# Kernel tuning notes

Measured on AMD Instinct MI355X. Metric: run time of the kernel, lower is better.

The kernel has to match this reference:

```python
import jax, jax.numpy as jnp
import numpy as np

FACTOR = 3   # ProbAttention factor hardcoded in Informer.__init__
N_HEADS = 8


def _ln(x, g, b, eps=1e-5):
    m = x.mean(-1, keepdims=True)
    v = ((x - m) ** 2).mean(-1, keepdims=True)
    return (x - m) / jnp.sqrt(v + eps) * g + b


def _pos_emb(L, d_model):
    # standard fixed sinusoidal positional embedding (Informer PositionalEmbedding)
    pos = np.arange(L, dtype=np.float32)[:, None]
    div = np.exp(np.arange(0, d_model, 2, dtype=np.float32) * (-np.log(10000.0) / d_model))
    pe = np.zeros((L, d_model), np.float32)
    pe[:, 0::2] = np.sin(pos * div)
    pe[:, 1::2] = np.cos(pos * div)
    return jnp.asarray(pe)


def _prob_attention(q, k, v, rng_key):
    # q,k,v: [B, L, H, D]; mask_flag=False, scale=None -> 1/sqrt(D)
    B, L, H, D = q.shape
    Q = q.transpose(0, 2, 1, 3)
    K = k.transpose(0, 2, 1, 3)
    V = v.transpose(0, 2, 1, 3)
    L_Q = L_K = L
    U_part = min(FACTOR * int(np.ceil(np.log(L_K))), L_K)   # sampled keys per query
    u = min(FACTOR * int(np.ceil(np.log(L_Q))), L_Q)        # top queries kept
    # sample keys (shared across batch/heads, as in torch.randint(L_K,(L_Q,sample_k)))
    idx_sample = jax.random.randint(rng_key, (L_Q, U_part), 0, L_K)
    K_sample = K[:, :, idx_sample, :]                        # [B,H,L_Q,U_part,D]
    QK_sample = jnp.einsum('bhld,bhlsd->bhls', Q, K_sample)  # [B,H,L_Q,U_part]
    M = QK_sample.max(-1) - QK_sample.sum(-1) / L_K          # sparsity measure [B,H,L_Q]
    _, idx_top = jax.lax.top_k(M, u)                         # [B,H,u]
    Q_reduce = jnp.take_along_axis(Q, idx_top[..., None], axis=2)          # [B,H,u,D]
    scores = jnp.einsum('bhud,bhkd->bhuk', Q_reduce, K) / jnp.sqrt(jnp.float32(D))
    attn = jax.nn.softmax(scores, axis=-1)
    upd = jnp.einsum('bhuk,bhkd->bhud', attn, V)             # [B,H,u,D]
    # initial context = mean over values (mask_flag=False), overwrite at top queries
    ctx = jnp.broadcast_to(V.mean(axis=2, keepdims=True), (B, H, L_Q, D))
    bI = jnp.arange(B)[:, None, None]
    hI = jnp.arange(H)[None, :, None]
    ctx = ctx.at[bI, hI, idx_top].set(upd)
    return ctx.transpose(0, 2, 1, 3).reshape(B, L, H * D)


def _forward(x, time_features, g_in, b_in, W_tok, W_time, b_time,
             Wq, bq, Wk, bk, Wv, bv, Wo, bo, W1, b1, W2, b2,
             g1, be1, g2, be2, g_enc, b_enc, W_pre, b_pre, W_fc, b_fc):
    B, L, _ = x.shape
    d_model = W_tok.shape[-1]
    H = N_HEADS
    D = d_model // H
    x = _ln(x, g_in, b_in)                                   # input_norm over enc_in
    # DataEmbedding: circular Conv1d(k=3) token emb + positional + timeF linear
    xp = jnp.pad(x, ((0, 0), (1, 1), (0, 0)), mode='wrap')
    tok = jax.lax.conv_general_dilated(xp, W_tok, (1,), 'VALID',
                                       dimension_numbers=('NWC', 'WIO', 'NWC'))
    h = tok + _pos_emb(L, d_model)[None] + time_features @ W_time.T + b_time
    key = jax.random.key(42)
    for i in range(Wq.shape[0]):                              # e_layers (small, fixed)
        q = (h @ Wq[i].T + bq[i]).reshape(B, L, H, D)
        k = (h @ Wk[i].T + bk[i]).reshape(B, L, H, D)
        v = (h @ Wv[i].T + bv[i]).reshape(B, L, H, D)
        attn_out = _prob_attention(q, k, v, jax.random.fold_in(key, i))
        h = h + attn_out @ Wo[i].T + bo[i]
        h = _ln(h, g1[i], be1[i])
        y = jax.nn.relu(h @ W1[i].T + b1[i]) @ W2[i].T + b2[i]  # 1x1 convs == linears
        h = _ln(h + y, g2[i], be2[i])
    h = _ln(h, g_enc, b_enc)
    last = h[:, -1, :]
    return jax.nn.relu(last @ W_pre.T + b_pre) @ W_fc.T + b_fc


def setup_inputs() -> dict:
    key = jax.random.key(0)
    B, L, C_IN, DM, DFF, E = 8, 2048, 32, 512, 2048, 2
    ks = iter(jax.random.split(key, 48))

    def p(shape, s=0.02):
        return jax.random.normal(next(ks), shape, jnp.float32) * s

    return {
        'x': jax.random.normal(next(ks), (B, L, C_IN), jnp.float32),
        'time_features': jax.random.uniform(next(ks), (B, L, 4), jnp.float32),
        'g_in': jnp.ones((C_IN,), jnp.float32), 'b_in': jnp.zeros((C_IN,), jnp.float32),
        'W_tok': p((3, C_IN, DM)),
        'W_time': p((DM, 4)), 'b_time': jnp.zeros((DM,), jnp.float32),
        'Wq': p((E, DM, DM)), 'bq': jnp.zeros((E, DM), jnp.float32),
        'Wk': p((E, DM, DM)), 'bk': jnp.zeros((E, DM), jnp.float32),
        'Wv': p((E, DM, DM)), 'bv': jnp.zeros((E, DM), jnp.float32),
        'Wo': p((E, DM, DM)), 'bo': jnp.zeros((E, DM), jnp.float32),
        'W1': p((E, DFF, DM)), 'b1': jnp.zeros((E, DFF), jnp.float32),
        'W2': p((E, DM, DFF)), 'b2': jnp.zeros((E, DM), jnp.float32),
        'g1': jnp.ones((E, DM), jnp.float32), 'be1': jnp.zeros((E, DM), jnp.float32),
        'g2': jnp.ones((E, DM), jnp.float32), 'be2': jnp.zeros((E, DM), jnp.float32),
        'g_enc': jnp.ones((DM,), jnp.float32), 'b_enc': jnp.zeros((DM,), jnp.float32),
        'W_pre': p((DM // 2, DM)), 'b_pre': jnp.zeros((DM // 2,), jnp.float32),
        'W_fc': p((1, DM // 2)), 'b_fc': jnp.zeros((1,), jnp.float32),
    }


def reference(x, time_features, g_in, b_in, W_tok, W_time, b_time,
              Wq, bq, Wk, bk, Wv, bv, Wo, bo, W1, b1, W2, b2,
              g1, be1, g2, be2, g_enc, b_enc, W_pre, b_pre, W_fc, b_fc):
    return _forward(x, time_features, g_in, b_in, W_tok, W_time, b_time,
                    Wq, bq, Wk, bk, Wv, bv, Wo, bo, W1, b1, W2, b2,
                    g1, be1, g2, be2, g_enc, b_enc, W_pre, b_pre, W_fc, b_fc)
```

## Files before the change

kernel.cpp:

```cpp
#include <hip/hip_runtime.h>
#include <math.h>

#define BATCH 8
#define SEQ   2048
#define TOK   (BATCH*SEQ)
#define CIN   32
#define DM    512
#define DFF   2048
#define NH    8
#define HD    64
#define NSAMP 24
#define NTOP  24
#define EPS   1e-5f
#define QKVLD 1536

typedef unsigned int u32;
typedef unsigned short u16;
typedef unsigned long long u64;
typedef __attribute__((ext_vector_type(8))) short short8;
typedef __attribute__((ext_vector_type(4))) short short4v;
typedef __attribute__((ext_vector_type(4))) float floatx4;

__device__ __forceinline__ void async16(const void* g, void* l) {
    __builtin_amdgcn_global_load_lds((const __attribute__((address_space(1))) u32*)g,
                                     (__attribute__((address_space(3))) u32*)l, 16, 0, 0);
}
__device__ __forceinline__ u16 bf16rn(float f) {
    u32 u = __float_as_uint(f);
    return (u16)((u + 0x7fffu + ((u >> 16) & 1u)) >> 16);
}
__device__ __forceinline__ void sep_store(u16* base, size_t row, int ld2, int j, float v) {
    u16 hb = bf16rn(v);
    float r = v - __uint_as_float((u32)hb << 16);
    size_t o = row * (size_t)ld2 + (size_t)((j >> 3) << 4) + (j & 7);
    base[o] = hb;
    base[o + 8] = bf16rn(r);
}
__device__ __forceinline__ float sep_load(const u16* base, size_t row, int ld2, int j) {
    size_t o = row * (size_t)ld2 + (size_t)((j >> 3) << 4) + (j & 7);
    return __uint_as_float((u32)base[o] << 16) + __uint_as_float((u32)base[o + 8] << 16);
}
__device__ __forceinline__ float hl2f(u16 h, u16 l) {
    return __uint_as_float((u32)h << 16) + __uint_as_float((u32)l << 16);
}

__device__ __forceinline__ void tf_round(unsigned &x0, unsigned &x1, int r) {
    x0 += x1;
    x1 = (x1 << r) | (x1 >> (32 - r));
    x1 ^= x0;
}
__device__ __forceinline__ void threefry(unsigned k0, unsigned k1,
                                         unsigned c0, unsigned c1,
                                         unsigned &o0, unsigned &o1) {
    unsigned ks0 = k0, ks1 = k1, ks2 = k0 ^ k1 ^ 0x1BD11BDAu;
    unsigned x0 = c0 + ks0, x1 = c1 + ks1;
    tf_round(x0,x1,13); tf_round(x0,x1,15); tf_round(x0,x1,26); tf_round(x0,x1,6);
    x0 += ks1; x1 += ks2 + 1u;
    tf_round(x0,x1,17); tf_round(x0,x1,29); tf_round(x0,x1,16); tf_round(x0,x1,24);
    x0 += ks2; x1 += ks0 + 2u;
    tf_round(x0,x1,13); tf_round(x0,x1,15); tf_round(x0,x1,26); tf_round(x0,x1,6);
    x0 += ks0; x1 += ks1 + 3u;
    tf_round(x0,x1,17); tf_round(x0,x1,29); tf_round(x0,x1,16); tf_round(x0,x1,24);
    x0 += ks1; x1 += ks2 + 4u;
    tf_round(x0,x1,13); tf_round(x0,x1,15); tf_round(x0,x1,26); tf_round(x0,x1,6);
    x0 += ks2; x1 += ks0 + 5u;
    o0 = x0; o1 = x1;
}

__global__ void sample_kernel(int* __restrict__ idx_sample) {
    const int HALF = (SEQ * NSAMP) / 2;
    int p = blockIdx.x * blockDim.x + threadIdx.x;
    int li = blockIdx.y;
    if (p >= HALF) return;
    unsigned f0, f1;
    threefry(0u, 42u, 0u, (unsigned)li, f0, f1);
    unsigned a0, a1, b0, b1;
    threefry(f0, f1, 0u, 2u, a0, a1);
    threefry(f0, f1, 1u, 3u, b0, b1);
    unsigned o0, o1;
    threefry(a1, b1, (unsigned)p, (unsigned)(p + HALF), o0, o1);
    idx_sample[li * SEQ * NSAMP + p]        = (int)(o0 & (SEQ - 1));
    idx_sample[li * SEQ * NSAMP + p + HALF] = (int)(o1 & (SEQ - 1));
}

__global__ __launch_bounds__(256) void ln_in_kernel(const float* __restrict__ x,
        const float* __restrict__ g, const float* __restrict__ b,
        float* __restrict__ out) {
    int t = blockIdx.x * blockDim.x + threadIdx.x;
    if (t >= TOK) return;
    const float* xr = x + (size_t)t * CIN;
    float vals[CIN];
    float s = 0.f;
#pragma unroll
    for (int c = 0; c < CIN; c++) { vals[c] = xr[c]; s += vals[c]; }
    float m = s * (1.f / CIN);
    float v = 0.f;
#pragma unroll
    for (int c = 0; c < CIN; c++) { float d = vals[c] - m; v += d * d; }
    v *= (1.f / CIN);
    float inv = rsqrtf(v + EPS);
    float* orow = out + (size_t)t * CIN;
#pragma unroll
    for (int c = 0; c < CIN; c++) orow[c] = (vals[c] - m) * inv * g[c] + b[c];
}

__global__ __launch_bounds__(128) void im2col_kernel(const float* __restrict__ xln,
        u16* __restrict__ a) {
    int t = blockIdx.x;
    int j = threadIdx.x;
    if (j >= 96) return;
    int b = t >> 11, l = t & 2047;
    int w = j >> 5, c = j & 31;
    int lw = (l - 1 + w + SEQ) & 2047;
    sep_store(a, (size_t)t, 192, j, xln[(((size_t)b << 11) | lw) * CIN + c]);
}

__global__ __launch_bounds__(256) void wtok_split(const float* __restrict__ Wtok,
        u16* __restrict__ wt) {
    int e = blockIdx.x * 256 + threadIdx.x;
    int o = e / 96, j = e % 96;
    sep_store(wt, (size_t)o, 192, j, Wtok[(size_t)j * DM + o]);
}

__global__ __launch_bounds__(256) void pe_kernel(float* __restrict__ pe) {
    int e = blockIdx.x * 256 + threadIdx.x;
    int l = e >> 9, o = e & 511;
    const float c1 = -0.017988946039016f;
    int i2 = o & ~1;
    float div = expf((float)i2 * c1);
    float arg = (float)l * div;
    pe[e] = (o & 1) ? cosf(arg) : sinf(arg);
}

__global__ __launch_bounds__(256) void rsd_kernel(const float* __restrict__ pe,
        const float* __restrict__ tfeat, const float* __restrict__ Wtime,
        u16* __restrict__ rsd) {
    int t = blockIdx.x, tid = threadIdx.x;
    int l = t & 2047;
    float t0 = tfeat[(size_t)t * 4], t1 = tfeat[(size_t)t * 4 + 1];
    float t2 = tfeat[(size_t)t * 4 + 2], t3 = tfeat[(size_t)t * 4 + 3];
    for (int o = tid; o < DM; o += 256) {
        float v = pe[l * DM + o]
            + t0 * Wtime[o * 4] + t1 * Wtime[o * 4 + 1]
            + t2 * Wtime[o * 4 + 2] + t3 * Wtime[o * 4 + 3];
        sep_store(rsd, (size_t)t, 1024, o, v);
    }
}

__global__ __launch_bounds__(256) void split_weights(const float* __restrict__ Wq,
        const float* __restrict__ Wk, const float* __restrict__ Wv,
        const float* __restrict__ Wo, const float* __restrict__ W1,
        const float* __restrict__ W2, u16* __restrict__ out,
        const float* __restrict__ bq, const float* __restrict__ bk,
        const float* __restrict__ bv, float* __restrict__ bqkv) {
    int i = blockIdx.x * 256 + threadIdx.x;
    if (i < 1536)
        bqkv[i] = (i < 512) ? bq[i] : (i < 1024) ? bk[i - 512] : bv[i - 1024];
    if (i < 1048576) {
        const float* src = (i < 262144) ? Wq : (i < 524288) ? Wk : (i < 786432) ? Wv : Wo;
        int off = i & 262143;
        size_t base = (size_t)(i >> 18) * 524288;
        sep_store(out + base, (size_t)(off >> 9), 1024, off & 511, src[off]);
    } else if (i < 2097152) {
        int off = i - 1048576;
        sep_store(out + 2097152, (size_t)(off >> 9), 1024, off & 511, W1[off]);
    } else {
        int off = i - 2097152;
        sep_store(out + 4194304, (size_t)(off >> 11), 4096, off & 2047, W2[off]);
    }
}

template<bool RELU, bool RESP, bool OUTP, bool OUTB>
__global__ __launch_bounds__(256, 2) void gemm_pp(const u16* __restrict__ Ap,
        const u16* __restrict__ Wp, const float* __restrict__ bias,
        const u16* __restrict__ RsdS, float* __restrict__ Cf, u16* __restrict__ Cp,
        int ldc, int K, int lda) {
    __shared__ alignas(16) u16 At[2][8192];
    __shared__ alignas(16) u16 Wt[2][8192];
    const int tid = threadIdx.x;
    int linear = blockIdx.y * gridDim.x + blockIdx.x;
    int xcd = linear & 7, sseq = linear >> 3;
    int mper = gridDim.y >> 3;
    int mt = xcd * mper + (sseq % mper);
    int nt = sseq / mper;
    const int m0 = mt * 128, n0 = nt * 128;
    const int lane = tid & 63, wv = tid >> 6;
    const int wm = wv >> 1, wn = wv & 1;
    const int fr = lane & 15, q = lane >> 4;

    floatx4 acc[4][4] = {};

    const int r0 = tid >> 3;
    const int gc = (tid & 7) ^ (r0 & 7);
    const u16* abase = Ap + (size_t)(m0 + r0) * (2 * lda) + gc * 8;
    const u16* wbase = Wp + (size_t)(n0 + r0) * (2 * K) + gc * 8;
    const size_t astep = (size_t)32 * 2 * lda;
    const size_t wstep = (size_t)32 * 2 * K;
    const int doff = tid * 16;
    const int nk = K >> 5;

    const int cph = ((q << 1) ^ (fr & 7)) << 3;
    const int cpl = ((q << 1) ^ (fr & 7) ^ 1) << 3;

#pragma unroll
    for (int i = 0; i < 4; i++) {
        async16(abase + i * astep, (char*)At[0] + doff + i * 4096);
        async16(wbase + i * wstep, (char*)Wt[0] + doff + i * 4096);
    }

    for (int k = 0; k < nk; k++) {
        const int b = k & 1;
        __syncthreads();
        if (k + 1 < nk) {
            int k2 = (k + 1) << 6;
#pragma unroll
            for (int i = 0; i < 4; i++) {
                async16(abase + k2 + i * astep, (char*)At[b ^ 1] + doff + i * 4096);
                async16(wbase + k2 + i * wstep, (char*)Wt[b ^ 1] + doff + i * 4096);
            }
        }
        short8 ah[4], al[4];
#pragma unroll
        for (int mi = 0; mi < 4; mi++) {
            int r = wm * 64 + mi * 16 + fr;
            ah[mi] = *(const short8*)&At[b][r * 64 + cph];
            al[mi] = *(const short8*)&At[b][r * 64 + cpl];
        }
#pragma unroll
        for (int ni = 0; ni < 4; ni++) {
            int r = wn * 64 + ni * 16 + fr;
            short8 wh8 = *(const short8*)&Wt[b][r * 64 + cph];
            short8 wl8 = *(const short8*)&Wt[b][r * 64 + cpl];
#pragma unroll
            for (int mi = 0; mi < 4; mi++) {
                acc[mi][ni] = __builtin_amdgcn_mfma_f32_16x16x32_bf16(ah[mi], wh8, acc[mi][ni], 0, 0, 0);
                acc[mi][ni] = __builtin_amdgcn_mfma_f32_16x16x32_bf16(ah[mi], wl8, acc[mi][ni], 0, 0, 0);
                acc[mi][ni] = __builtin_amdgcn_mfma_f32_16x16x32_bf16(al[mi], wh8, acc[mi][ni], 0, 0, 0);
            }
        }
    }
#pragma unroll
    for (int ni = 0; ni < 4; ni++) {
        int col = n0 + wn * 64 + ni * 16 + fr;
        float bv = bias[col];
#pragma unroll
        for (int mi = 0; mi < 4; mi++) {
            int row = m0 + wm * 64 + mi * 16 + q * 4;
#pragma unroll
            for (int r = 0; r < 4; r++) {
                float v = acc[mi][ni][r] + bv;
                if (RESP) v += sep_load(RsdS, (size_t)(row + r), 2 * ldc, col);
                if (RELU) v = fmaxf(v, 0.f);
                if (OUTP)      sep_store(Cp, (size_t)(row + r), 2 * ldc, col, v);
                else if (OUTB) Cp[(size_t)(row + r) * ldc + col] = bf16rn(v);
                else           Cf[(size_t)(row + r) * ldc + col] = v;
            }
        }
    }
}

template<bool RELU, bool RESP>
__global__ __launch_bounds__(256, 2) void gemm_sb(const u16* __restrict__ Ab,
        const u16* __restrict__ Wp, const float* __restrict__ bias,
        const u16* __restrict__ RsdS, float* __restrict__ Cf,
        int ldc, int K, int lda) {
    __shared__ alignas(16) u16 At[2][4096];
    __shared__ alignas(16) u16 Wt[2][8192];
    const int tid = threadIdx.x;
    int linear = blockIdx.y * gridDim.x + blockIdx.x;
    int xcd = linear & 7, sseq = linear >> 3;
    int mper = gridDim.y >> 3;
    int mt = xcd * mper + (sseq % mper);
    int nt = sseq / mper;
    const int m0 = mt * 128, n0 = nt * 128;
    const int lane = tid & 63, wv = tid >> 6;
    const int wm = wv >> 1, wn = wv & 1;
    const int fr = lane & 15, q = lane >> 4;

    floatx4 acc[4][4] = {};

    const int ar = tid & 127;
    const u16* abase = Ab + (size_t)(m0 + ar) * lda + (tid >> 7) * 8;
    const int adoff = tid * 16;
    const int r0 = tid >> 3;
    const int gc = (tid & 7) ^ (r0 & 7);
    const u16* wbase = Wp + (size_t)(n0 + r0) * (2 * K) + gc * 8;
    const size_t wstep = (size_t)32 * 2 * K;
    const int wdoff = tid * 16;
    const int nk = K >> 5;

    const int cph = ((q << 1) ^ (fr & 7)) << 3;
    const int cpl = ((q << 1) ^ (fr & 7) ^ 1) << 3;

#pragma unroll
    for (int i = 0; i < 2; i++)
        async16(abase + i * 16, (char*)At[0] + adoff + i * 4096);
#pragma unroll
    for (int i = 0; i < 4; i++)
        async16(wbase + i * wstep, (char*)Wt[0] + wdoff + i * 4096);

    for (int k = 0; k < nk; k++) {
        const int b = k & 1;
        __syncthreads();
        if (k + 1 < nk) {
            int ka = (k + 1) << 5;
            int kw = (k + 1) << 6;
#pragma unroll
            for (int i = 0; i < 2; i++)
                async16(abase + ka + i * 16, (char*)At[b ^ 1] + adoff + i * 4096);
#pragma unroll
            for (int i = 0; i < 4; i++)
                async16(wbase + kw + i * wstep, (char*)Wt[b ^ 1] + wdoff + i * 4096);
        }
        short8 af[4];
#pragma unroll
        for (int mi = 0; mi < 4; mi++) {
            int r = wm * 64 + mi * 16 + fr;
            af[mi] = *(const short8*)&At[b][q * 1024 + r * 8];
        }
#pragma unroll
        for (int ni = 0; ni < 4; ni++) {
            int r = wn * 64 + ni * 16 + fr;
            short8 wh8 = *(const short8*)&Wt[b][r * 64 + cph];
            short8 wl8 = *(const short8*)&Wt[b][r * 64 + cpl];
#pragma unroll
            for (int mi = 0; mi < 4; mi++) {
                acc[mi][ni] = __builtin_amdgcn_mfma_f32_16x16x32_bf16(af[mi], wh8, acc[mi][ni], 0, 0, 0);
                acc[mi][ni] = __builtin_amdgcn_mfma_f32_16x16x32_bf16(af[mi], wl8, acc[mi][ni], 0, 0, 0);
            }
        }
    }
#pragma unroll
    for (int ni = 0; ni < 4; ni++) {
        int col = n0 + wn * 64 + ni * 16 + fr;
        float bv = bias[col];
#pragma unroll
        for (int mi = 0; mi < 4; mi++) {
            int row = m0 + wm * 64 + mi * 16 + q * 4;
#pragma unroll
            for (int r = 0; r < 4; r++) {
                float v = acc[mi][ni][r] + bv;
                if (RESP) v += sep_load(RsdS, (size_t)(row + r), 2 * ldc, col);
                if (RELU) v = fmaxf(v, 0.f);
                Cf[(size_t)(row + r) * ldc + col] = v;
            }
        }
    }
}

__global__ __launch_bounds__(256) void qk_sample_kernel(const float* __restrict__ qkv,
        const int* __restrict__ idx_sample, float* __restrict__ Mout) {
    int r = (blockIdx.x * 256 + threadIdx.x) >> 6;
    int lane = threadIdx.x & 63;
    if (r >= BATCH * NH * SEQ) return;
    int b = r / (NH * SEQ);
    int head = (r / SEQ) % NH;
    int l = r % SEQ;
    int sidx = lane >> 4, dc = lane & 15;
    const float* qrow = qkv + ((size_t)(b * SEQ + l)) * QKVLD + head * HD + dc * 4;
    float4 qf = *(const float4*)qrow;
    int myidx = (lane < NSAMP) ? idx_sample[l * NSAMP + lane] : 0;
    const float* kbase = qkv + (size_t)b * SEQ * QKVLD + 512 + head * HD + dc * 4;
    int kidx[6];
#pragma unroll
    for (int p = 0; p < 6; p++) kidx[p] = __shfl(myidx, p * 4 + sidx);
    float4 kf[6];
#pragma unroll
    for (int p = 0; p < 6; p++) kf[p] = *(const float4*)(kbase + (size_t)kidx[p] * QKVLD);
    float mx = -INFINITY, sm = 0.f;
#pragma unroll
    for (int p = 0; p < 6; p++) {
        float part = qf.x * kf[p].x + qf.y * kf[p].y + qf.z * kf[p].z + qf.w * kf[p].w;
        part += __shfl_xor(part, 1);
        part += __shfl_xor(part, 2);
        part += __shfl_xor(part, 4);
        part += __shfl_xor(part, 8);
        mx = fmaxf(mx, part);
        sm += part;
    }
    mx = fmaxf(mx, __shfl_xor(mx, 16));
    mx = fmaxf(mx, __shfl_xor(mx, 32));
    sm += __shfl_xor(sm, 16);
    sm += __shfl_xor(sm, 32);
    if (lane == 0) Mout[r] = mx - sm * (1.f / SEQ);
}

__device__ __forceinline__ u64 pack_key(float v, int idx) {
    u32 u = __float_as_uint(v);
    u32 m = (u & 0x80000000u) ? ~u : (u | 0x80000000u);
    return ((u64)m << 32) | (u32)(~(u32)idx);
}

__global__ __launch_bounds__(256) void topk_part(const float* __restrict__ Mbuf,
        u64* __restrict__ cand) {
    __shared__ u64 wred[4];
    int bh = blockIdx.x, chunk = blockIdx.y;
    int tid = threadIdx.x, wv = tid >> 6, lane = tid & 63;
    int l = chunk * 256 + tid;
    u64 val = pack_key(Mbuf[(size_t)bh * SEQ + l], l);
    for (int it = 0; it < NTOP; it++) {
        u64 w = val;
#pragma unroll
        for (int off = 32; off > 0; off >>= 1) {
            u64 o = __shfl_xor(w, off);
            if (o > w) w = o;
        }
        if (lane == 0) wred[wv] = w;
        __syncthreads();
        u64 win = wred[0];
        if (wred[1] > win) win = wred[1];
        if (wred[2] > win) win = wred[2];
        if (wred[3] > win) win = wred[3];
        if (val == win) val = 0;
        if (tid == 0) cand[((size_t)bh * 8 + chunk) * NTOP + it] = win;
        __syncthreads();
    }
}

__global__ __launch_bounds__(256) void topk_merge(const u64* __restrict__ cand,
        int* __restrict__ idx_top) {
    __shared__ u64 wred[4];
    int bh = blockIdx.x;
    int tid = threadIdx.x, wv = tid >> 6, lane = tid & 63;
    u64 val = (tid < 8 * NTOP) ? cand[(size_t)bh * 8 * NTOP + tid] : 0;
    for (int it = 0; it < NTOP; it++) {
        u64 w = val;
#pragma unroll
        for (int off = 32; off > 0; off >>= 1) {
            u64 o = __shfl_xor(w, off);
            if (o > w) w = o;
        }
        if (lane == 0) wred[wv] = w;
        __syncthreads();
        u64 win = wred[0];
        if (wred[1] > win) win = wred[1];
        if (wred[2] > win) win = wred[2];
        if (wred[3] > win) win = wred[3];
        if (val == win) val = 0;
        if (tid == 0) idx_top[bh * NTOP + it] = (int)(~(u32)(win & 0xffffffffull) & (SEQ - 1));
        __syncthreads();
    }
}

__global__ __launch_bounds__(256) void vmean_kernel(const float* __restrict__ qkv,
        float* __restrict__ vmean) {
    __shared__ float red[256];
    int bh = blockIdx.x, slab = blockIdx.y;
    int b = bh >> 3, head = bh & 7;
    int seg = threadIdx.x >> 6, d = threadIdx.x & 63;
    int base_row = slab * 256 + seg * 64;
    float s = 0.f;
    for (int r = 0; r < 64; r++)
        s += qkv[((size_t)(b * SEQ + base_row + r)) * QKVLD + 1024 + head * HD + d];
    red[threadIdx.x] = s;
    __syncthreads();
    if (threadIdx.x < 128) red[threadIdx.x] += red[threadIdx.x + 128];
    __syncthreads();
    if (threadIdx.x < 64) {
        float t = red[threadIdx.x] + red[threadIdx.x + 64];
        atomicAdd(&vmean[bh * HD + d], t * (1.f / SEQ));
    }
}

__global__ void fillctx_kernel(const float* __restrict__ vmean, u16* __restrict__ out) {
    int e = blockIdx.x * 256 + threadIdx.x;
    int t = e >> 6, g = e & 63;
    const float* vm = vmean + ((((t >> 11) << 3) | (g >> 3)) << 6) + (g & 7) * 8;
    short8 hh, ll;
#pragma unroll
    for (int s = 0; s < 8; s++) {
        float v = vm[s];
        u16 hb = bf16rn(v);
        hh[s] = (short)hb;
        ll[s] = (short)bf16rn(v - __uint_as_float((u32)hb << 16));
    }
    u16* dp = out + (size_t)t * 1024 + g * 16;
    *(short8*)dp = hh;
    *(short8*)(dp + 8) = ll;
}

__global__ __launch_bounds__(256) void spattn_flash(const float* __restrict__ qkv,
        const int* __restrict__ idx_top, float* __restrict__ opart,
        float* __restrict__ mspart) {
    __shared__ float KtT[64][65];
    __shared__ float Vt[64][65];
    __shared__ float Qs[24][64];
    __shared__ float Ps[24][66];
    int bh = blockIdx.x, slab = blockIdx.y;
    int b = bh >> 3, h = bh & 7;
    int tid = threadIdx.x;
    int wv = tid >> 6, lane = tid & 63;
    for (int i = tid; i < NTOP * 64; i += 256) {
        int u = i >> 6, d = i & 63;
        int qi = idx_top[bh * NTOP + u];
        Qs[u][d] = qkv[((size_t)(b * SEQ + qi)) * QKVLD + h * HD + d];
    }
    float m[6], s[6], o[6], alpha[6];
#pragma unroll
    for (int j = 0; j < 6; j++) { m[j] = -INFINITY; s[j] = 0.f; o[j] = 0.f; }
    int key0 = slab * 512;
    int sr = tid >> 2, sc0 = (tid & 3) * 16;
    for (int t = 0; t < 8; t++) {
        int kbase = key0 + t * 64;
        __syncthreads();
        const float* kr = qkv + ((size_t)(b * SEQ + kbase + sr)) * QKVLD + 512 + h * HD + sc0;
        const float* vr = qkv + ((size_t)(b * SEQ + kbase + sr)) * QKVLD + 1024 + h * HD + sc0;
        float kf[16], vf[16];
        *(float4*)&kf[0]  = *(const float4*)(kr);
        *(float4*)&kf[4]  = *(const float4*)(kr + 4);
        *(float4*)&kf[8]  = *(const float4*)(kr + 8);
        *(float4*)&kf[12] = *(const float4*)(kr + 12);
        *(float4*)&vf[0]  = *(const float4*)(vr);
        *(float4*)&vf[4]  = *(const float4*)(vr + 4);
        *(float4*)&vf[8]  = *(const float4*)(vr + 8);
        *(float4*)&vf[12] = *(const float4*)(vr + 12);
#pragma unroll
        for (int i = 0; i < 16; i++) {
            KtT[sc0 + i][sr] = kf[i];
            Vt[sr][sc0 + i] = vf[i];
        }
        __syncthreads();
        float dot[6] = {};
#pragma unroll
        for (int d = 0; d < 64; d++) {
            float kv = KtT[d][lane];
#pragma unroll
            for (int j = 0; j < 6; j++) dot[j] += Qs[wv * 6 + j][d] * kv;
        }
#pragma unroll
        for (int j = 0; j < 6; j++) {
            float sc = dot[j] * 0.125f;
            float tmax = sc;
            for (int off = 32; off > 0; off >>= 1) tmax = fmaxf(tmax, __shfl_xor(tmax, off));
            float mn = fmaxf(m[j], tmax);
            float p = __expf(sc - mn);
            float psum = p;
            for (int off = 32; off > 0; off >>= 1) psum += __shfl_xor(psum, off);
            alpha[j] = __expf(m[j] - mn);
            s[j] = s[j] * alpha[j] + psum;
            m[j] = mn;
            Ps[wv * 6 + j][lane] = p;
        }
        float pv[6] = {};
#pragma unroll
        for (int key = 0; key < 64; key++) {
            float vvv = Vt[key][lane];
#pragma unroll
            for (int j = 0; j < 6; j++) pv[j] += Ps[wv * 6 + j][key] * vvv;
        }
#pragma unroll
        for (int j = 0; j < 6; j++) o[j] = o[j] * alpha[j] + pv[j];
    }
    float* ob = opart + ((size_t)(bh * 4 + slab)) * NTOP * 64;
#pragma unroll
    for (int j = 0; j < 6; j++) ob[(wv * 6 + j) * 64 + lane] = o[j];
    if (lane == 0) {
        float* ms = mspart + ((size_t)(bh * 4 + slab)) * NTOP * 2;
#pragma unroll
        for (int j = 0; j < 6; j++) {
            ms[(wv * 6 + j) * 2]     = m[j];
            ms[(wv * 6 + j) * 2 + 1] = s[j];
        }
    }
}

__global__ __launch_bounds__(256) void spattn_combine(const float* __restrict__ opart,
        const float* __restrict__ mspart, const int* __restrict__ idx_top,
        u16* __restrict__ out) {
    __shared__ float wgt[4][NTOP];
    int bh = blockIdx.x;
    int b = bh >> 3, h = bh & 7;
    int tid = threadIdx.x;
    if (tid < NTOP) {
        float mv[4], sv[4];
        float M = -INFINITY;
#pragma unroll
        for (int sl = 0; sl < 4; sl++) {
            mv[sl] = mspart[((size_t)(bh * 4 + sl)) * NTOP * 2 + tid * 2];
            sv[sl] = mspart[((size_t)(bh * 4 + sl)) * NTOP * 2 + tid * 2 + 1];
            M = fmaxf(M, mv[sl]);
        }
        float S = 0.f;
#pragma unroll
        for (int sl = 0; sl < 4; sl++) S += sv[sl] * __expf(mv[sl] - M);
        float invS = 1.f / S;
#pragma unroll
        for (int sl = 0; sl < 4; sl++) wgt[sl][tid] = __expf(mv[sl] - M) * invS;
    }
    __syncthreads();
    for (int i = tid; i < NTOP * 64; i += 256) {
        int u = i >> 6, d = i & 63;
        float val = 0.f;
#pragma unroll
        for (int sl = 0; sl < 4; sl++)
            val += wgt[sl][u] * opart[(((size_t)(bh * 4 + sl)) * NTOP + u) * 64 + d];
        int qi = idx_top[bh * NTOP + u];
        sep_store(out, (size_t)(b * SEQ + qi), 1024, h * HD + d, val);
    }
}

template<bool INP, bool OUTSEP>
__global__ __launch_bounds__(256) void ln_kernel(const float* __restrict__ srcF,
        const u16* __restrict__ srcS, const float* __restrict__ g,
        const float* __restrict__ b, float* __restrict__ dstF, u16* __restrict__ dstS) {
    int wv = threadIdx.x >> 6, lane = threadIdx.x & 63;
    int t = blockIdx.x * 4 + wv;
    float xv[8];
    if (INP) {
        const u16* sp = srcS + (size_t)t * 1024 + (lane >> 1) * 16 + (lane & 1) * 4;
        short4v h0 = *(const short4v*)sp;
        short4v l0 = *(const short4v*)(sp + 8);
        short4v h1 = *(const short4v*)(sp + 512);
        short4v l1 = *(const short4v*)(sp + 520);
#pragma unroll
        for (int i = 0; i < 4; i++) {
            xv[i]     = hl2f((u16)h0[i], (u16)l0[i]);
            xv[i + 4] = hl2f((u16)h1[i], (u16)l1[i]);
        }
    } else {
        float4 x0 = *(const float4*)&srcF[(size_t)t * DM + lane * 4];
        float4 x1 = *(const float4*)&srcF[(size_t)t * DM + lane * 4 + 256];
        xv[0] = x0.x; xv[1] = x0.y; xv[2] = x0.z; xv[3] = x0.w;
        xv[4] = x1.x; xv[5] = x1.y; xv[6] = x1.z; xv[7] = x1.w;
    }
    float s = 0.f, s2 = 0.f;
#pragma unroll
    for (int i = 0; i < 8; i++) { s += xv[i]; s2 += xv[i] * xv[i]; }
#pragma unroll
    for (int off = 32; off > 0; off >>= 1) {
        s  += __shfl_xor(s, off);
        s2 += __shfl_xor(s2, off);
    }
    float m = s * (1.f / DM);
    float var = s2 * (1.f / DM) - m * m;
    float inv = rsqrtf(var + EPS);
    float4 g0 = *(const float4*)&g[lane * 4];
    float4 g1 = *(const float4*)&g[lane * 4 + 256];
    float4 b0 = *(const float4*)&b[lane * 4];
    float4 b1 = *(const float4*)&b[lane * 4 + 256];
    float y[8];
    y[0] = (xv[0] - m) * inv * g0.x + b0.x;  y[1] = (xv[1] - m) * inv * g0.y + b0.y;
    y[2] = (xv[2] - m) * inv * g0.z + b0.z;  y[3] = (xv[3] - m) * inv * g0.w + b0.w;
    y[4] = (xv[4] - m) * inv * g1.x + b1.x;  y[5] = (xv[5] - m) * inv * g1.y + b1.y;
    y[6] = (xv[6] - m) * inv * g1.z + b1.z;  y[7] = (xv[7] - m) * inv * g1.w + b1.w;
    if (OUTSEP) {
        u16* dp = dstS + (size_t)t * 1024 + (lane >> 1) * 16 + (lane & 1) * 4;
        short4v hh0, ll0, hh1, ll1;
#pragma unroll
        for (int i = 0; i < 4; i++) {
            u16 hb = bf16rn(y[i]);
            hh0[i] = (short)hb;
            ll0[i] = (short)bf16rn(y[i] - __uint_as_float((u32)hb << 16));
            u16 hb2 = bf16rn(y[i + 4]);
            hh1[i] = (short)hb2;
            ll1[i] = (short)bf16rn(y[i + 4] - __uint_as_float((u32)hb2 << 16));
        }
        *(short4v*)dp = hh0;
        *(short4v*)(dp + 8) = ll0;
        *(short4v*)(dp + 512) = hh1;
        *(short4v*)(dp + 520) = ll1;
    } else {
        float4 o0 = { y[0], y[1], y[2], y[3] };
        float4 o1 = { y[4], y[5], y[6], y[7] };
        *(float4*)&dstF[(size_t)t * DM + lane * 4] = o0;
        *(float4*)&dstF[(size_t)t * DM + lane * 4 + 256] = o1;
    }
}

__global__ __launch_bounds__(256) void head_kernel(const float* __restrict__ hfin,
        const float* __restrict__ Wpre, const float* __restrict__ bpre,
        const float* __restrict__ Wfc, const float* __restrict__ bfc,
        float* __restrict__ out) {
    __shared__ float last[DM];
    __shared__ float red[256];
    int b = blockIdx.x, tid = threadIdx.x;
    const float* hr = hfin + ((size_t)(b * SEQ + SEQ - 1)) * DM;
    last[tid] = hr[tid];
    last[tid + 256] = hr[tid + 256];
    __syncthreads();
    float acc = bpre[tid];
    for (int c = 0; c < DM; c++) acc += last[c] * Wpre[tid * DM + c];
    acc = fmaxf(acc, 0.f);
    red[tid] = acc * Wfc[tid];
    __syncthreads();
    for (int s = 128; s > 0; s >>= 1) { if (tid < s) red[tid] += red[tid + s]; __syncthreads(); }
    if (tid == 0) out[b] = red[0] + bfc[0];
}

extern "C" void kernel_launch(void* const* d_in, const int* in_sizes, int n_in,
                              void* d_out, int out_size, void* d_ws, size_t ws_size,
                              hipStream_t stream) {
    (void)in_sizes; (void)n_in; (void)out_size; (void)ws_size;
    const float* x      = (const float*)d_in[0];
    const float* tfeat  = (const float*)d_in[1];
    const float* g_in   = (const float*)d_in[2];
    const float* b_in   = (const float*)d_in[3];
    const float* W_tok  = (const float*)d_in[4];
    const float* W_time = (const float*)d_in[5];
    const float* b_time = (const float*)d_in[6];
    const float* Wq     = (const float*)d_in[7];
    const float* bq     = (const float*)d_in[8];
    const float* Wk     = (const float*)d_in[9];
    const float* bk     = (const float*)d_in[10];
    const float* Wv     = (const float*)d_in[11];
    const float* bv     = (const float*)d_in[12];
    const float* Wo     = (const float*)d_in[13];
    const float* bo     = (const float*)d_in[14];
    const float* W1     = (const float*)d_in[15];
    const float* b1     = (const float*)d_in[16];
    const float* W2     = (const float*)d_in[17];
    const float* b2     = (const float*)d_in[18];
    const float* g1     = (const float*)d_in[19];
    const float* be1    = (const float*)d_in[20];
    const float* g2     = (const float*)d_in[21];
    const float* be2    = (const float*)d_in[22];
    const float* g_enc  = (const float*)d_in[23];
    const float* b_enc  = (const float*)d_in[24];
    const float* W_pre  = (const float*)d_in[25];
    const float* b_pre  = (const float*)d_in[26];
    const float* W_fc   = (const float*)d_in[27];
    const float* b_fc   = (const float*)d_in[28];
    float* out = (float*)d_out;

    char* ws = (char*)d_ws;
    u16*   hp   = (u16*)(ws);
    float* hf   = (float*)(ws + 33554432);
    char*  bigc = ws + 67108864;
    float* qkv  = (float*)bigc;
    u16*   ctxP = (u16*)(bigc + 100663296);
    u16*   midP = (u16*)bigc;
    u16*   midB = (u16*)bigc;
    float* xln  = (float*)(bigc);
    u16*   acvP = (u16*)(bigc + 2097152);
    float* pe   = (float*)(bigc + 8388608);
    u16*   rsdS = (u16*)(bigc + 12582912);
    u16*   wtok = (u16*)(bigc + 46137344);
    u16*   wsep       = (u16*)(ws + 201326592);
    float* Mbuf       = (float*)(ws + 213909504);
    float* vmean      = (float*)(ws + 214433792);
    int*   idx_sample = (int*)(ws + 214450176);
    int*   idx_top    = (int*)(ws + 214843392);
    float* biasqkv    = (float*)(ws + 214849536);
    u64*   cand       = (u64*)(ws + 214855680);
    float* opart      = (float*)(ws + 214953984);
    float* mspart     = (float*)(ws + 216526848);

    ln_in_kernel<<<TOK / 256, 256, 0, stream>>>(x, g_in, b_in, xln);
    im2col_kernel<<<TOK, 128, 0, stream>>>(xln, acvP);
    wtok_split<<<192, 256, 0, stream>>>(W_tok, wtok);
    pe_kernel<<<4096, 256, 0, stream>>>(pe);
    rsd_kernel<<<TOK, 256, 0, stream>>>(pe, tfeat, W_time, rsdS);
    sample_kernel<<<dim3(96, 2), 256, 0, stream>>>(idx_sample);

    gemm_pp<false, true, true, false><<<dim3(4, 128), 256, 0, stream>>>(
        acvP, wtok, b_time, rsdS, nullptr, hp, DM, 96, 96);

    const u16* wqkv_p = wsep;
    const u16* wo_p = wsep + 1572864;
    const u16* w1_p = wsep + 2097152;
    const u16* w2_p = wsep + 4194304;

    for (int li = 0; li < 2; li++) {
        split_weights<<<12288, 256, 0, stream>>>(
            Wq + (size_t)li * DM * DM, Wk + (size_t)li * DM * DM,
            Wv + (size_t)li * DM * DM, Wo + (size_t)li * DM * DM,
            W1 + (size_t)li * DFF * DM, W2 + (size_t)li * DM * DFF, wsep,
            bq + (size_t)li * DM, bk + (size_t)li * DM, bv + (size_t)li * DM, biasqkv);

        const float* bo_i = bo + (size_t)li * DM;
        const float* b1_i = b1 + (size_t)li * DFF;
        const float* b2_i = b2 + (size_t)li * DM;
        const float* g1_i = g1 + (size_t)li * DM;
        const float* be1_i = be1 + (size_t)li * DM;
        const float* g2_i = g2 + (size_t)li * DM;
        const float* be2_i = be2 + (size_t)li * DM;

        gemm_pp<false, false, false, false><<<dim3(QKVLD / 128, TOK / 128), 256, 0, stream>>>(
            hp, wqkv_p, biasqkv, nullptr, qkv, nullptr, QKVLD, DM, DM);

        qk_sample_kernel<<<(BATCH * NH * SEQ) / 4, 256, 0, stream>>>(
            qkv, idx_sample + li * SEQ * NSAMP, Mbuf);
        topk_part<<<dim3(BATCH * NH, 8), 256, 0, stream>>>(Mbuf, cand);
        topk_merge<<<BATCH * NH, 256, 0, stream>>>(cand, idx_top);
        hipMemsetAsync(vmean, 0, BATCH * NH * HD * sizeof(float), stream);
        vmean_kernel<<<dim3(BATCH * NH, 8), 256, 0, stream>>>(qkv, vmean);
        fillctx_kernel<<<(TOK * 64) / 256, 256, 0, stream>>>(vmean, ctxP);
        spattn_flash<<<dim3(BATCH * NH, 4), 256, 0, stream>>>(qkv, idx_top, opart, mspart);
        spattn_combine<<<BATCH * NH, 256, 0, stream>>>(opart, mspart, idx_top, ctxP);

        gemm_pp<false, true, false, false><<<dim3(DM / 128, TOK / 128), 256, 0, stream>>>(
            ctxP, wo_p, bo_i, hp, hf, nullptr, DM, DM, DM);
        ln_kernel<false, true><<<TOK / 4, 256, 0, stream>>>(hf, nullptr, g1_i, be1_i, nullptr, hp);

        if (li == 0) {
            gemm_pp<true, false, true, false><<<dim3(DFF / 128, TOK / 128), 256, 0, stream>>>(
                hp, w1_p, b1_i, nullptr, nullptr, midP, DFF, DM, DM);
            gemm_pp<false, true, false, false><<<dim3(DM / 128, TOK / 128), 256, 0, stream>>>(
                midP, w2_p, b2_i, hp, hf, nullptr, DM, DFF, DFF);
        } else {
            gemm_pp<true, false, false, true><<<dim3(DFF / 128, TOK / 128), 256, 0, stream>>>(
                hp, w1_p, b1_i, nullptr, nullptr, midB, DFF, DM, DM);
            gemm_sb<false, true><<<dim3(DM / 128, TOK / 128), 256, 0, stream>>>(
                midB, w2_p, b2_i, hp, hf, DM, DFF, DFF);
        }
        ln_kernel<false, true><<<TOK / 4, 256, 0, stream>>>(hf, nullptr, g2_i, be2_i, nullptr, hp);
    }

    ln_kernel<true, false><<<TOK / 4, 256, 0, stream>>>(nullptr, hp, g_enc, b_enc, hf, nullptr);
    head_kernel<<<BATCH, 256, 0, stream>>>(hf, W_pre, b_pre, W_fc, b_fc, out);
}
```

Baseline: 1.122 ms.

## Add 8-wave triple-buffered split-bf16 GEMM with XCD-aware tile mapping

Introduces gemm8, a 512-thread GEMM with 256x128 or 128x256 tiles. It triple-buffers LDS via async global-to-LDS loads, interleaves the next-stage weight loads between MFMA groups, and raises wave priority during MFMA bursts. Block indices are remapped so each XCD handles a contiguous band of M tiles, which should improve L2 reuse. Most projection and FFN GEMMs switch to it, at the cost of more LDS per block, extra barriers, and fewer blocks for the smaller GEMMs.

```diff
diff --git a/kernel.cpp b/kernel.cpp
--- a/kernel.cpp
+++ b/kernel.cpp
@@ -239,6 +239,151 @@
             }
         }
     }
+#pragma unroll
+    for (int ni = 0; ni < 4; ni++) {
+        int col = n0 + wn * 64 + ni * 16 + fr;
+        float bv = bias[col];
+#pragma unroll
+        for (int mi = 0; mi < 4; mi++) {
+            int row = m0 + wm * 64 + mi * 16 + q * 4;
+#pragma unroll
+            for (int r = 0; r < 4; r++) {
+                float v = acc[mi][ni][r] + bv;
+                if (RESP) v += sep_load(RsdS, (size_t)(row + r), 2 * ldc, col);
+                if (RELU) v = fmaxf(v, 0.f);
+                if (OUTP)      sep_store(Cp, (size_t)(row + r), 2 * ldc, col, v);
+                else if (OUTB) Cp[(size_t)(row + r) * ldc + col] = bf16rn(v);
+                else           Cf[(size_t)(row + r) * ldc + col] = v;
+            }
+        }
+    }
+}
+
+template<int CFG, bool RELU, bool RESP, bool OUTP, bool OUTB>
+__global__ __launch_bounds__(512, 2) void gemm8(const u16* __restrict__ Ap,
+        const u16* __restrict__ Wp, const float* __restrict__ bias,
+        const u16* __restrict__ RsdS, float* __restrict__ Cf, u16* __restrict__ Cp,
+        int ldc, int K, int lda) {
+    constexpr int BM = CFG ? 256 : 128;
+    constexpr int BN = CFG ? 128 : 256;
+    constexpr int NA = BM / 64;
+    constexpr int NW = BN / 64;
+    __shared__ alignas(16) u16 As[3][BM * 64];
+    __shared__ alignas(16) u16 Ws[3][BN * 64];
+    const int tid = threadIdx.x;
+    int linear = blockIdx.y * gridDim.x + blockIdx.x;
+    int xcd = linear & 7, sseq = linear >> 3;
+    int mper = gridDim.y >> 3;
+    int mt = xcd * mper + (sseq % mper);
+    int nt = sseq / mper;
+    const int m0 = mt * BM, n0 = nt * BN;
+    const int lane = tid & 63, wv = tid >> 6;
+    const int wm = CFG ? (wv >> 1) : (wv >> 2);
+    const int wn = CFG ? (wv & 1) : (wv & 3);
+    const int fr = lane & 15, q = lane >> 4;
+
+    floatx4 acc[4][4] = {};
+
+    const int r0 = tid >> 3;
+    const int gc = (tid & 7) ^ (r0 & 7);
+    const u16* abase = Ap + (size_t)(m0 + r0) * (2 * lda) + gc * 8;
+    const u16* wbase = Wp + (size_t)(n0 + r0) * (2 * K) + gc * 8;
+    const size_t astep = (size_t)64 * 2 * lda;
+    const size_t wstep = (size_t)64 * 2 * K;
+    const int doff = tid * 16;
+    const int nk = K >> 5;
+
+    const int cph = ((q << 1) ^ (fr & 7)) << 3;
+    const int cpl = cph ^ 8;
+
+#pragma unroll
+    for (int i = 0; i < NA; i++) async16(abase + i * astep, (char*)As[0] + doff + i * 8192);
+#pragma unroll
+    for (int i = 0; i < NW; i++) async16(wbase + i * wstep, (char*)Ws[0] + doff + i * 8192);
+#pragma unroll
+    for (int i = 0; i < NA; i++) async16(abase + 64 + i * astep, (char*)As[1] + doff + i * 8192);
+#pragma unroll
+    for (int i = 0; i < NW; i++) async16(wbase + 64 + i * wstep, (char*)Ws[1] + doff + i * 8192);
+    asm volatile("s_waitcnt vmcnt(6)" ::: "memory");
+    __builtin_amdgcn_s_barrier();
+
+    int cur = 0;
+    for (int k = 0; k < nk; k++) {
+        const u16* Ab = As[cur];
+        const u16* Wb = Ws[cur];
+        int nxt = cur + 2; if (nxt >= 3) nxt -= 3;
+        const bool stage = (k + 2) < nk;
+        const int ko = (k + 2) << 6;
+
+        short8 ah[4], al[4];
+#pragma unroll
+        for (int mi = 0; mi < 4; mi++) {
+            int r = wm * 64 + mi * 16 + fr;
+            ah[mi] = *(const short8*)&Ab[r * 64 + cph];
+            al[mi] = *(const short8*)&Ab[r * 64 + cpl];
+        }
+        short8 wh, wl;
+        {
+            int r = wn * 64 + fr;
+            wh = *(const short8*)&Wb[r * 64 + cph];
+            wl = *(const short8*)&Wb[r * 64 + cpl];
+        }
+        if (stage) {
+#pragma unroll
+            for (int i = 0; i < NA; i++)
+                async16(abase + ko + i * astep, (char*)As[nxt] + doff + i * 8192);
+        }
+        __builtin_amdgcn_s_barrier();
+        asm volatile("s_waitcnt lgkmcnt(0)" ::: "memory");
+        __builtin_amdgcn_sched_barrier(0);
+        __builtin_amdgcn_s_setprio(1);
+#pragma unroll
+        for (int mi = 0; mi < 4; mi++) {
+            acc[mi][0] = __builtin_amdgcn_mfma_f32_16x16x32_bf16(ah[mi], wh, acc[mi][0], 0, 0, 0);
+            acc[mi][0] = __builtin_amdgcn_mfma_f32_16x16x32_bf16(ah[mi], wl, acc[mi][0], 0, 0, 0);
+            acc[mi][0] = __builtin_amdgcn_mfma_f32_16x16x32_bf16(al[mi], wh, acc[mi][0], 0, 0, 0);
+        }
+        __builtin_amdgcn_s_setprio(0);
+        __builtin_amdgcn_s_barrier();
+
+#pragma unroll
+        for (int ni = 1; ni < 4; ni++) {
+            int r = wn * 64 + ni * 16 + fr;
+            wh = *(const short8*)&Wb[r * 64 + cph];
+            wl = *(const short8*)&Wb[r * 64 + cpl];
+            if (stage) {
+                if (ni == 1) {
+#pragma unroll
+                    for (int i = 0; i < NW / 2; i++)
+                        async16(wbase + ko + i * wstep, (char*)Ws[nxt] + doff + i * 8192);
+                } else if (ni == 2) {
+#pragma unroll
+                    for (int i = NW / 2; i < NW; i++)
+                        async16(wbase + ko + i * wstep, (char*)Ws[nxt] + doff + i * 8192);
+                }
+            }
+            __builtin_amdgcn_s_barrier();
+            asm volatile("s_waitcnt lgkmcnt(0)" ::: "memory");
+            __builtin_amdgcn_sched_barrier(0);
+            __builtin_amdgcn_s_setprio(1);
+#pragma unroll
+            for (int mi = 0; mi < 4; mi++) {
+                acc[mi][ni] = __builtin_amdgcn_mfma_f32_16x16x32_bf16(ah[mi], wh, acc[mi][ni], 0, 0, 0);
+                acc[mi][ni] = __builtin_amdgcn_mfma_f32_16x16x32_bf16(ah[mi], wl, acc[mi][ni], 0, 0, 0);
+                acc[mi][ni] = __builtin_amdgcn_mfma_f32_16x16x32_bf16(al[mi], wh, acc[mi][ni], 0, 0, 0);
+            }
+            __builtin_amdgcn_s_setprio(0);
+            __builtin_amdgcn_s_barrier();
+        }
+
+        if (k + 1 < nk) {
+            if (k + 2 < nk) asm volatile("s_waitcnt vmcnt(6)" ::: "memory");
+            else            asm volatile("s_waitcnt vmcnt(0)" ::: "memory");
+            __builtin_amdgcn_s_barrier();
+        }
+        cur++; if (cur == 3) cur = 0;
+    }
+
 #pragma unroll
     for (int ni = 0; ni < 4; ni++) {
         int col = n0 + wn * 64 + ni * 16 + fr;
@@ -775,7 +920,7 @@
         const float* g2_i = g2 + (size_t)li * DM;
         const float* be2_i = be2 + (size_t)li * DM;
 
-        gemm_pp<false, false, false, false><<<dim3(QKVLD / 128, TOK / 128), 256, 0, stream>>>(
+        gemm8<0, false, false, false, false><<<dim3(QKVLD / 256, TOK / 128), 512, 0, stream>>>(
             hp, wqkv_p, biasqkv, nullptr, qkv, nullptr, QKVLD, DM, DM);
 
         qk_sample_kernel<<<(BATCH * NH * SEQ) / 4, 256, 0, stream>>>(
@@ -788,17 +933,17 @@
         spattn_flash<<<dim3(BATCH * NH, 4), 256, 0, stream>>>(qkv, idx_top, opart, mspart);
         spattn_combine<<<BATCH * NH, 256, 0, stream>>>(opart, mspart, idx_top, ctxP);
 
-        gemm_pp<false, true, false, false><<<dim3(DM / 128, TOK / 128), 256, 0, stream>>>(
+        gemm8<1, false, true, false, false><<<dim3(DM / 128, TOK / 256), 512, 0, stream>>>(
             ctxP, wo_p, bo_i, hp, hf, nullptr, DM, DM, DM);
         ln_kernel<false, true><<<TOK / 4, 256, 0, stream>>>(hf, nullptr, g1_i, be1_i, nullptr, hp);
 
         if (li == 0) {
-            gemm_pp<true, false, true, false><<<dim3(DFF / 128, TOK / 128), 256, 0, stream>>>(
+            gemm8<0, true, false, true, false><<<dim3(DFF / 256, TOK / 128), 512, 0, stream>>>(
                 hp, w1_p, b1_i, nullptr, nullptr, midP, DFF, DM, DM);
-            gemm_pp<false, true, false, false><<<dim3(DM / 128, TOK / 128), 256, 0, stream>>>(
+            gemm8<1, false, true, false, false><<<dim3(DM / 128, TOK / 256), 512, 0, stream>>>(
                 midP, w2_p, b2_i, hp, hf, nullptr, DM, DFF, DFF);
         } else {
-            gemm_pp<true, false, false, true><<<dim3(DFF / 128, TOK / 128), 256, 0, stream>>>(
+            gemm8<0, true, false, false, true><<<dim3(DFF / 256, TOK / 128), 512, 0, stream>>>(
                 hp, w1_p, b1_i, nullptr, nullptr, midB, DFF, DM, DM);
             gemm_sb<false, true><<<dim3(DM / 128, TOK / 128), 256, 0, stream>>>(
                 midB, w2_p, b2_i, hp, hf, DM, DFF, DFF);
```

After: 1.267 ms. 1.13x slower.

## Replace output projection GEMM with per-batch default row plus sparse top-query corrections

Applied to the files above, without the earlier changes.

The context tensor is the per-(batch,head) value mean everywhere except at 24 top queries per head. So the output projection is computed once per batch as Wo·vmean+bo, broadcast into the residual, and then corrected with rank-limited Wo·(upd−vmean) updates, applied atomically only at the selected rows. This removes the dense TOK×512×512 Wo GEMM and the fill of the context buffer. It also doubles the key slabs in the sparse flash attention to raise parallelism. In exchange it relies on fp32 atomics into hf and uses the fp32 Wo directly instead of the split-bf16 path, which changes the numerics slightly.

```diff
diff --git a/kernel.cpp b/kernel.cpp
--- a/kernel.cpp
+++ b/kernel.cpp
@@ -11,6 +11,7 @@
 #define HD    64
 #define NSAMP 24
 #define NTOP  24
+#define NSLAB 8
 #define EPS   1e-5f
 #define QKVLD 1536
 
@@ -462,21 +463,75 @@
     }
 }
 
-__global__ void fillctx_kernel(const float* __restrict__ vmean, u16* __restrict__ out) {
-    int e = blockIdx.x * 256 + threadIdx.x;
-    int t = e >> 6, g = e & 63;
-    const float* vm = vmean + ((((t >> 11) << 3) | (g >> 3)) << 6) + (g & 7) * 8;
-    short8 hh, ll;
-#pragma unroll
-    for (int s = 0; s < 8; s++) {
-        float v = vm[s];
-        u16 hb = bf16rn(v);
-        hh[s] = (short)hb;
-        ll[s] = (short)bf16rn(v - __uint_as_float((u32)hb << 16));
-    }
-    u16* dp = out + (size_t)t * 1024 + g * 16;
-    *(short8*)dp = hh;
-    *(short8*)(dp + 8) = ll;
+__global__ __launch_bounds__(512) void ydef_kernel(const float* __restrict__ Wo,
+        const float* __restrict__ bo, const float* __restrict__ vmean,
+        float* __restrict__ ydef) {
+    __shared__ float vm[DM];
+    int b = blockIdx.x, o = threadIdx.x;
+    vm[o] = vmean[b * DM + o];
+    __syncthreads();
+    const float* wr = Wo + (size_t)o * DM;
+    float acc = bo[o];
+    for (int j = 0; j < DM; j += 4) {
+        float4 w4 = *(const float4*)&wr[j];
+        acc += w4.x * vm[j] + w4.y * vm[j + 1] + w4.z * vm[j + 2] + w4.w * vm[j + 3];
+    }
+    ydef[b * DM + o] = acc;
+}
+
+__global__ __launch_bounds__(256) void resid_kernel(const u16* __restrict__ hp,
+        const float* __restrict__ ydef, float* __restrict__ hf) {
+    int wv = threadIdx.x >> 6, lane = threadIdx.x & 63;
+    int t = blockIdx.x * 4 + wv;
+    int b = t >> 11;
+    const u16* sp = hp + (size_t)t * 1024 + (lane >> 1) * 16 + (lane & 1) * 4;
+    short4v h0 = *(const short4v*)sp;
+    short4v l0 = *(const short4v*)(sp + 8);
+    short4v h1 = *(const short4v*)(sp + 512);
+    short4v l1 = *(const short4v*)(sp + 520);
+    int j0 = (lane >> 1) * 8 + (lane & 1) * 4;
+    const float* yd = ydef + b * DM;
+    float4 y0 = *(const float4*)&yd[j0];
+    float4 y1 = *(const float4*)&yd[j0 + 256];
+    float4 o0, o1;
+    o0.x = hl2f((u16)h0[0], (u16)l0[0]) + y0.x;
+    o0.y = hl2f((u16)h0[1], (u16)l0[1]) + y0.y;
+    o0.z = hl2f((u16)h0[2], (u16)l0[2]) + y0.z;
+    o0.w = hl2f((u16)h0[3], (u16)l0[3]) + y0.w;
+    o1.x = hl2f((u16)h1[0], (u16)l1[0]) + y1.x;
+    o1.y = hl2f((u16)h1[1], (u16)l1[1]) + y1.y;
+    o1.z = hl2f((u16)h1[2], (u16)l1[2]) + y1.z;
+    o1.w = hl2f((u16)h1[3], (u16)l1[3]) + y1.w;
+    *(float4*)&hf[(size_t)t * DM + j0] = o0;
+    *(float4*)&hf[(size_t)t * DM + j0 + 256] = o1;
+}
+
+__global__ __launch_bounds__(512) void corr_kernel(const float* __restrict__ Wo,
+        const float* __restrict__ updC, const float* __restrict__ vmean,
+        const int* __restrict__ idx_top, float* __restrict__ hf) {
+    __shared__ float delta[NTOP][HD];
+    __shared__ int rows[NTOP];
+    int bh = blockIdx.x, b = bh >> 3, h = bh & 7;
+    int tid = threadIdx.x;
+    for (int i = tid; i < NTOP * HD; i += 512) {
+        int u = i >> 6, d = i & 63;
+        delta[u][d] = updC[((size_t)bh * NTOP + u) * HD + d] - vmean[bh * HD + d];
+    }
+    if (tid < NTOP) rows[tid] = idx_top[bh * NTOP + tid];
+    __syncthreads();
+    float w[HD];
+    const float* wr = Wo + (size_t)tid * DM + h * HD;
+#pragma unroll
+    for (int d = 0; d < HD; d += 4) {
+        float4 f = *(const float4*)&wr[d];
+        w[d] = f.x; w[d + 1] = f.y; w[d + 2] = f.z; w[d + 3] = f.w;
+    }
+    for (int u = 0; u < NTOP; u++) {
+        float acc = 0.f;
+#pragma unroll
+        for (int d = 0; d < HD; d++) acc += w[d] * delta[u][d];
+        atomicAdd(&hf[(size_t)(b * SEQ + rows[u]) * DM + tid], acc);
+    }
 }
 
 __global__ __launch_bounds__(256) void spattn_flash(const float* __restrict__ qkv,
@@ -498,9 +553,9 @@
     float m[6], s[6], o[6], alpha[6];
 #pragma unroll
     for (int j = 0; j < 6; j++) { m[j] = -INFINITY; s[j] = 0.f; o[j] = 0.f; }
-    int key0 = slab * 512;
+    int key0 = slab * (SEQ / NSLAB);
     int sr = tid >> 2, sc0 = (tid & 3) * 16;
-    for (int t = 0; t < 8; t++) {
+    for (int t = 0; t < (SEQ / NSLAB) / 64; t++) {
         int kbase = key0 + t * 64;
         __syncthreads();
         const float* kr = qkv + ((size_t)(b * SEQ + kbase + sr)) * QKVLD + 512 + h * HD + sc0;
@@ -551,11 +606,11 @@
 #pragma unroll
         for (int j = 0; j < 6; j++) o[j] = o[j] * alpha[j] + pv[j];
     }
-    float* ob = opart + ((size_t)(bh * 4 + slab)) * NTOP * 64;
+    float* ob = opart + ((size_t)(bh * NSLAB + slab)) * NTOP * 64;
 #pragma unroll
     for (int j = 0; j < 6; j++) ob[(wv * 6 + j) * 64 + lane] = o[j];
     if (lane == 0) {
-        float* ms = mspart + ((size_t)(bh * 4 + slab)) * NTOP * 2;
+        float* ms = mspart + ((size_t)(bh * NSLAB + slab)) * NTOP * 2;
 #pragma unroll
         for (int j = 0; j < 6; j++) {
             ms[(wv * 6 + j) * 2]     = m[j];
@@ -565,37 +620,34 @@
 }
 
 __global__ __launch_bounds__(256) void spattn_combine(const float* __restrict__ opart,
-        const float* __restrict__ mspart, const int* __restrict__ idx_top,
-        u16* __restrict__ out) {
-    __shared__ float wgt[4][NTOP];
+        const float* __restrict__ mspart, float* __restrict__ updC) {
+    __shared__ float wgt[NSLAB][NTOP];
     int bh = blockIdx.x;
-    int b = bh >> 3, h = bh & 7;
     int tid = threadIdx.x;
     if (tid < NTOP) {
-        float mv[4], sv[4];
+        float mv[NSLAB], sv[NSLAB];
         float M = -INFINITY;
 #pragma unroll
-        for (int sl = 0; sl < 4; sl++) {
-            mv[sl] = mspart[((size_t)(bh * 4 + sl)) * NTOP * 2 + tid * 2];
-            sv[sl] = mspart[((size_t)(bh * 4 + sl)) * NTOP * 2 + tid * 2 + 1];
+        for (int sl = 0; sl < NSLAB; sl++) {
+            mv[sl] = mspart[((size_t)(bh * NSLAB + sl)) * NTOP * 2 + tid * 2];
+            sv[sl] = mspart[((size_t)(bh * NSLAB + sl)) * NTOP * 2 + tid * 2 + 1];
             M = fmaxf(M, mv[sl]);
         }
         float S = 0.f;
 #pragma unroll
-        for (int sl = 0; sl < 4; sl++) S += sv[sl] * __expf(mv[sl] - M);
+        for (int sl = 0; sl < NSLAB; sl++) S += sv[sl] * __expf(mv[sl] - M);
         float invS = 1.f / S;
 #pragma unroll
-        for (int sl = 0; sl < 4; sl++) wgt[sl][tid] = __expf(mv[sl] - M) * invS;
+        for (int sl = 0; sl < NSLAB; sl++) wgt[sl][tid] = __expf(mv[sl] - M) * invS;
     }
     __syncthreads();
     for (int i = tid; i < NTOP * 64; i += 256) {
         int u = i >> 6, d = i & 63;
         float val = 0.f;
 #pragma unroll
-        for (int sl = 0; sl < 4; sl++)
-            val += wgt[sl][u] * opart[(((size_t)(bh * 4 + sl)) * NTOP + u) * 64 + d];
-        int qi = idx_top[bh * NTOP + u];
-        sep_store(out, (size_t)(b * SEQ + qi), 1024, h * HD + d, val);
+        for (int sl = 0; sl < NSLAB; sl++)
+            val += wgt[sl][u] * opart[(((size_t)(bh * NSLAB + sl)) * NTOP + u) * 64 + d];
+        updC[((size_t)bh * NTOP + u) * 64 + d] = val;
     }
 }
 
@@ -727,9 +779,12 @@
     float* hf   = (float*)(ws + 33554432);
     char*  bigc = ws + 67108864;
     float* qkv  = (float*)bigc;
-    u16*   ctxP = (u16*)(bigc + 100663296);
     u16*   midP = (u16*)bigc;
     u16*   midB = (u16*)bigc;
+    float* updC   = (float*)(bigc + 100663296);
+    float* ydefb  = (float*)(bigc + 101056512);
+    float* opart  = (float*)(bigc + 101072896);
+    float* mspart = (float*)(bigc + 104218624);
     float* xln  = (float*)(bigc);
     u16*   acvP = (u16*)(bigc + 2097152);
     float* pe   = (float*)(bigc + 8388608);
@@ -742,8 +797,6 @@
     int*   idx_top    = (int*)(ws + 214843392);
     float* biasqkv    = (float*)(ws + 214849536);
     u64*   cand       = (u64*)(ws + 214855680);
-    float* opart      = (float*)(ws + 214953984);
-    float* mspart     = (float*)(ws + 216526848);
 
     ln_in_kernel<<<TOK / 256, 256, 0, stream>>>(x, g_in, b_in, xln);
     im2col_kernel<<<TOK, 128, 0, stream>>>(xln, acvP);
@@ -756,7 +809,6 @@
         acvP, wtok, b_time, rsdS, nullptr, hp, DM, 96, 96);
 
     const u16* wqkv_p = wsep;
-    const u16* wo_p = wsep + 1572864;
     const u16* w1_p = wsep + 2097152;
     const u16* w2_p = wsep + 4194304;
 
@@ -767,6 +819,7 @@
             W1 + (size_t)li * DFF * DM, W2 + (size_t)li * DM * DFF, wsep,
             bq + (size_t)li * DM, bk + (size_t)li * DM, bv + (size_t)li * DM, biasqkv);
 
+        const float* Wo_i = Wo + (size_t)li * DM * DM;
         const float* bo_i = bo + (size_t)li * DM;
         const float* b1_i = b1 + (size_t)li * DFF;
         const float* b2_i = b2 + (size_t)li * DM;
@@ -784,12 +837,12 @@
         topk_merge<<<BATCH * NH, 256, 0, stream>>>(cand, idx_top);
         hipMemsetAsync(vmean, 0, BATCH * NH * HD * sizeof(float), stream);
         vmean_kernel<<<dim3(BATCH * NH, 8), 256, 0, stream>>>(qkv, vmean);
-        fillctx_kernel<<<(TOK * 64) / 256, 256, 0, stream>>>(vmean, ctxP);
-        spattn_flash<<<dim3(BATCH * NH, 4), 256, 0, stream>>>(qkv, idx_top, opart, mspart);
-        spattn_combine<<<BATCH * NH, 256, 0, stream>>>(opart, mspart, idx_top, ctxP);
-
-        gemm_pp<false, true, false, false><<<dim3(DM / 128, TOK / 128), 256, 0, stream>>>(
-            ctxP, wo_p, bo_i, hp, hf, nullptr, DM, DM, DM);
+        ydef_kernel<<<BATCH, 512, 0, stream>>>(Wo_i, bo_i, vmean, ydefb);
+        spattn_flash<<<dim3(BATCH * NH, NSLAB), 256, 0, stream>>>(qkv, idx_top, opart, mspart);
+        spattn_combine<<<BATCH * NH, 256, 0, stream>>>(opart, mspart, updC);
+
+        resid_kernel<<<TOK / 4, 256, 0, stream>>>(hp, ydefb, hf);
+        corr_kernel<<<BATCH * NH, 512, 0, stream>>>(Wo_i, updC, vmean, idx_top, hf);
         ln_kernel<false, true><<<TOK / 4, 256, 0, stream>>>(hf, nullptr, g1_i, be1_i, nullptr, hp);
 
         if (li == 0) {
```

Result: no change. 1.131 ms (+0.8%).
